# Kernel tuning notes

Hardware: AMD Instinct MI355X
Metric: run time of the kernel (lower is better)

The kernel has to match this reference:

```python
import jax, jax.numpy as jnp
import numpy as np

E, D_IN, H, D_OUT = 8, 6, 32, 2
B = 1048576

def setup_inputs() -> dict:
    key = jax.random.key(0)
    ks = jax.random.split(key, 11)
    s = lambda *sh: 1.0 / np.sqrt(sh[-2])  # glorot-ish scale
    x = jax.random.normal(ks[0], (B, D_IN), dtype=jnp.float32)
    # stacked expert weights
    W1 = jax.random.normal(ks[1], (E, D_IN, H), dtype=jnp.float32) * (1.0/np.sqrt(D_IN))
    b1 = jnp.zeros((E, H), dtype=jnp.float32)
    W2 = jax.random.normal(ks[2], (E, H, H), dtype=jnp.float32) * (1.0/np.sqrt(H))
    b2 = jnp.zeros((E, H), dtype=jnp.float32)
    W3 = jax.random.normal(ks[3], (E, H, D_OUT), dtype=jnp.float32) * (1.0/np.sqrt(H))
    b3 = jnp.zeros((E, D_OUT), dtype=jnp.float32)
    # gating network
    Wg1 = jax.random.normal(ks[4], (D_IN, H), dtype=jnp.float32) * (1.0/np.sqrt(D_IN))
    bg1 = jnp.zeros((H,), dtype=jnp.float32)
    Wg2 = jax.random.normal(ks[5], (H, E), dtype=jnp.float32) * (1.0/np.sqrt(H))
    bg2 = jnp.zeros((E,), dtype=jnp.float32)
    return {"x": x, "W1": W1, "b1": b1, "W2": W2, "b2": b2, "W3": W3, "b3": b3,
            "Wg1": Wg1, "bg1": bg1, "Wg2": Wg2, "bg2": bg2}

def reference(x, W1, b1, W2, b2, W3, b3, Wg1, bg1, Wg2, bg2):
    # gate: [B, E] softmax probs
    g = jax.nn.softmax(jax.nn.relu(x @ Wg1 + bg1) @ Wg2 + bg2, axis=-1)
    # all experts as batched GEMMs: h1, h2 [B, E, H]; y [B, E, 2]
    h1 = jax.nn.relu(jnp.einsum('bd,edh->beh', x, W1) + b1)
    h2 = jax.nn.relu(jnp.einsum('beh,ehk->bek', h1, W2) + b2)
    y = jnp.einsum('beh,eho->beo', h2, W3) + b3
    # gate-weighted sum over experts -> [B, 2]
    return jnp.einsum('be,beo->bo', g, y)
```

## Files before the change

kernel.cpp:

```cpp
#include <hip/hip_runtime.h>


typedef _Float16 half2_t __attribute__((ext_vector_type(2)));
typedef _Float16 half4_t __attribute__((ext_vector_type(4)));
typedef _Float16 half8_t __attribute__((ext_vector_type(8)));
typedef __fp16   fp16v2  __attribute__((ext_vector_type(2)));
typedef float  float4_t __attribute__((ext_vector_type(4)));
typedef float  float2_t __attribute__((ext_vector_type(2)));
typedef int    int2_t   __attribute__((ext_vector_type(2)));
typedef int    int4_t   __attribute__((ext_vector_type(4)));

#define MFMA_K32(A, B, C) __builtin_amdgcn_mfma_f32_16x16x32_f16((A), (B), (C), 0, 0, 0)
#define MFMA_K16(A, B, C) __builtin_amdgcn_mfma_f32_16x16x16f16((A), (B), (C), 0, 0, 0)

static constexpr int E_ = 8, DIN_ = 6, H_ = 32, EPW_ = 2;

union H8U { half2_t h2[4]; half8_t h8; int4_t i4; };
union H4U { half2_t h2[2]; half4_t h4; int2_t i2; };
union HI  { half2_t h; int i; };
union PKU { fp16v2 p; half2_t h; };
union FI  { float f; int i; };

__device__ __forceinline__ half2_t pkrtz(float a, float b) {
    PKU u; u.p = __builtin_amdgcn_cvt_pkrtz(a, b);
    return u.h;
}

__device__ __forceinline__ half2_t relu2(half2_t v) {
    const half2_t z = {(_Float16)0.0f, (_Float16)0.0f};
    return __builtin_elementwise_max(v, z);
}

__device__ __forceinline__ float bperm_f(int addr, float v) {
    FI u; u.f = v;
    u.i = __builtin_amdgcn_ds_bpermute(addr, u.i);
    return u.f;
}

__global__ __launch_bounds__(256, 2)
void moe_kernel(
    const float* __restrict__ x,  const float* __restrict__ W1, const float* __restrict__ b1,
    const float* __restrict__ W2, const float* __restrict__ b2, const float* __restrict__ W3,
    const float* __restrict__ b3, const float* __restrict__ Wg1, const float* __restrict__ bg1,
    const float* __restrict__ Wg2, const float* __restrict__ bg2,
    float* __restrict__ out, int nTiles, int tilesPerBlock)
{
    const int tid  = threadIdx.x;
    const int lane = tid & 63;
    const int t    = lane & 15;
    const int q    = lane >> 4;
    const int wv   = tid >> 6;
    const int eb   = wv * EPW_;

    __shared__ float2_t cbuf[2][4][16];

    const float L2E = 1.44269504f;

    H4U G1[2];
    #pragma unroll
    for (int f = 0; f < 2; ++f) {
        float v0 = 0.f, v1 = 0.f, v2 = 0.f, v3 = 0.f;
        if (q == 0) {
            v0 = Wg1[0 * H_ + f * 16 + t]; v1 = Wg1[1 * H_ + f * 16 + t];
            v2 = Wg1[2 * H_ + f * 16 + t]; v3 = Wg1[3 * H_ + f * 16 + t];
        } else if (q == 1) {
            v0 = Wg1[4 * H_ + f * 16 + t]; v1 = Wg1[5 * H_ + f * 16 + t];
            v2 = bg1[f * 16 + t];          v3 = 0.f;
        }
        G1[f].h2[0] = pkrtz(v0, v1); G1[f].h2[1] = pkrtz(v2, v3);
    }
    H8U G2;
    #pragma unroll
    for (int p = 0; p < 4; ++p) {
        int c0 = ((p >> 1) << 4) + q * 4 + ((p & 1) << 1);
        float v0 = (t < E_) ? Wg2[c0 * E_ + t] * L2E : 0.f;
        float v1 = (t < E_) ? Wg2[(c0 + 1) * E_ + t] * L2E : 0.f;
        G2.h2[p] = pkrtz(v0, v1);
    }

    H4U W1F[EPW_][2];
    H8U W2F[EPW_][2], W3F[EPW_], B2R[EPW_];
    #pragma unroll
    for (int j = 0; j < EPW_; ++j) {
        const int e = eb + j;
        #pragma unroll
        for (int f = 0; f < 2; ++f) {
            float v0 = 0.f, v1 = 0.f, v2 = 0.f, v3 = 0.f;
            const float* We = W1 + (size_t)e * DIN_ * H_ + f * 16 + t;
            if (q == 0)      { v0 = We[0 * H_]; v1 = We[1 * H_]; v2 = We[2 * H_]; v3 = We[3 * H_]; }
            else if (q == 1) { v0 = We[4 * H_]; v1 = We[5 * H_]; v2 = b1[e * H_ + f * 16 + t]; }
            W1F[j][f].h2[0] = pkrtz(v0, v1); W1F[j][f].h2[1] = pkrtz(v2, v3);
        }
        #pragma unroll
        for (int p = 0; p < 4; ++p) {
            int c0 = ((p >> 1) << 4) + q * 4 + ((p & 1) << 1);
            W2F[j][0].h2[p] = pkrtz(W2[(e * H_ + c0) * H_ + 0  + t], W2[(e * H_ + c0 + 1) * H_ + 0  + t]);
            W2F[j][1].h2[p] = pkrtz(W2[(e * H_ + c0) * H_ + 16 + t], W2[(e * H_ + c0 + 1) * H_ + 16 + t]);
            B2R[j].h2[p]    = pkrtz(b2[e * H_ + c0], b2[e * H_ + c0 + 1]);
            float v0 = 0.f, v1 = 0.f;
            if ((t >> 1) == e) {
                v0 = W3[(e * H_ + c0) * 2 + (t & 1)];
                v1 = W3[(e * H_ + c0 + 1) * 2 + (t & 1)];
            }
            W3F[j].h2[p] = pkrtz(v0, v1);
        }
    }

    float4_t bg2F, b3F;
    #pragma unroll
    for (int r = 0; r < 4; ++r) {
        int m = q * 4 + r;
        bg2F[r] = (m < E_) ? bg2[m] * L2E : 0.f;
        b3F[r]  = b3[m];
    }
    const float4_t zero4 = {0.f, 0.f, 0.f, 0.f};

    const int gsrc = ((((q >> 1) << 4) | t) << 2);
    const int csrc = (((wv << 4) | t) << 2);

    const int tile0 = blockIdx.x * tilesPerBlock;

    const int xo1 = (q == 0) ? 0 : 4;
    const int xo2 = (q == 0) ? 2 : 4;
    const float* xq = x + ((size_t)tile0 * 16 + t) * DIN_;
    float2_t la = {0.f, 0.f}, lb = {0.f, 0.f};
    if (tile0 < nTiles) {
        la = *(const float2_t*)(xq + xo1);
        lb = *(const float2_t*)(xq + xo2);
    }

    HI onei; onei.h = pkrtz(1.f, 0.f);
    const bool isq0 = (q == 0);

    for (int it = 0; it < tilesPerBlock; ++it) {
        const int tile = tile0 + it;
        if (tile >= nTiles) break;

        H4U ux;
        ux.h2[0] = pkrtz(la[0], la[1]);
        HI hb; hb.h = pkrtz(lb[0], lb[1]);
        HI se; se.i = isq0 ? hb.i : onei.i;
        ux.h2[1] = se.h;
        const half4_t xB = ux.h4;

        if ((it + 1) < tilesPerBlock && (tile + 1) < nTiles) {
            const float* xn = xq + (size_t)(it + 1) * 16 * DIN_;
            la = *(const float2_t*)(xn + xo1);
            lb = *(const float2_t*)(xn + xo2);
        }

        float4_t hgLo = MFMA_K16(G1[0].h4, xB, zero4);
        float4_t hgHi = MFMA_K16(G1[1].h4, xB, zero4);
        H8U uh;
        uh.h2[0] = relu2(pkrtz(hgLo[0], hgLo[1]));
        uh.h2[1] = relu2(pkrtz(hgLo[2], hgLo[3]));
        uh.h2[2] = relu2(pkrtz(hgHi[0], hgHi[1]));
        uh.h2[3] = relu2(pkrtz(hgHi[2], hgHi[3]));
        float4_t gl = MFMA_K32(G2.h8, uh.h8, bg2F);

        float ex0 = __builtin_amdgcn_exp2f(gl[0]);
        float ex1 = __builtin_amdgcn_exp2f(gl[1]);
        float ex2 = __builtin_amdgcn_exp2f(gl[2]);
        float ex3 = __builtin_amdgcn_exp2f(gl[3]);
        float s = (ex0 + ex1) + (ex2 + ex3);
        s += __shfl_xor(s, 16);
        float rs = __builtin_amdgcn_rcpf(s);
        HI pa, pb;
        pa.h = pkrtz(ex0, ex1);
        pb.h = pkrtz(ex2, ex3);
        int va = __builtin_amdgcn_ds_bpermute(gsrc, pa.i);
        int vb = __builtin_amdgcn_ds_bpermute(gsrc, pb.i);
        HI gsel; gsel.i = (q & 1) ? vb : va;
        float ga = (float)gsel.h[0];
        float gb = (float)gsel.h[1];

        float4_t Y = b3F;
        #pragma unroll
        for (int j = 0; j < EPW_; ++j) {
            float4_t lo = MFMA_K16(W1F[j][0].h4, xB, zero4);
            float4_t hi = MFMA_K16(W1F[j][1].h4, xB, zero4);
            H8U u1;
            u1.h2[0] = relu2(pkrtz(lo[0], lo[1]));
            u1.h2[1] = relu2(pkrtz(lo[2], lo[3]));
            u1.h2[2] = relu2(pkrtz(hi[0], hi[1]));
            u1.h2[3] = relu2(pkrtz(hi[2], hi[3]));
            float4_t lo2 = MFMA_K32(W2F[j][0].h8, u1.h8, zero4);
            float4_t hi2 = MFMA_K32(W2F[j][1].h8, u1.h8, zero4);
            H8U u2;
            u2.h2[0] = relu2(pkrtz(lo2[0], lo2[1]) + B2R[j].h2[0]);
            u2.h2[1] = relu2(pkrtz(lo2[2], lo2[3]) + B2R[j].h2[1]);
            u2.h2[2] = relu2(pkrtz(hi2[0], hi2[1]) + B2R[j].h2[2]);
            u2.h2[3] = relu2(pkrtz(hi2[2], hi2[3]) + B2R[j].h2[3]);
            Y = MFMA_K32(W3F[j].h8, u2.h8, Y);
        }

        float p0 = ga * Y[0] + gb * Y[2];
        float p1 = ga * Y[1] + gb * Y[3];
        p0 = bperm_f(csrc, p0);
        p1 = bperm_f(csrc, p1);

        if (lane < 16) {
            float2_t o = {p0, p1};
            cbuf[it & 1][wv][t] = o;
        }
        __syncthreads();
        if (wv == 0 && lane < 16) {
            float2_t o  = cbuf[it & 1][0][t];
            float2_t o1 = cbuf[it & 1][1][t];
            float2_t o2 = cbuf[it & 1][2][t];
            float2_t o3 = cbuf[it & 1][3][t];
            o[0] = (o[0] + o1[0] + o2[0] + o3[0]) * rs;
            o[1] = (o[1] + o1[1] + o2[1] + o3[1]) * rs;
            *(float2_t*)(out + ((size_t)tile * 16 + t) * 2) = o;
        }
    }
}

extern "C" void kernel_launch(void* const* d_in, const int* in_sizes, int n_in,
                              void* d_out, int out_size, void* d_ws, size_t ws_size,
                              hipStream_t stream) {
    const float* x   = (const float*)d_in[0];
    const float* W1  = (const float*)d_in[1];
    const float* b1  = (const float*)d_in[2];
    const float* W2  = (const float*)d_in[3];
    const float* b2  = (const float*)d_in[4];
    const float* W3  = (const float*)d_in[5];
    const float* b3  = (const float*)d_in[6];
    const float* Wg1 = (const float*)d_in[7];
    const float* bg1 = (const float*)d_in[8];
    const float* Wg2 = (const float*)d_in[9];
    const float* bg2 = (const float*)d_in[10];
    float* out = (float*)d_out;

    const int B      = in_sizes[0] / DIN_;
    const int nTiles = (B + 15) / 16;
    const int blocks = 2048;
    const int tpb    = (nTiles + blocks - 1) / blocks;

    moe_kernel<<<blocks, 256, 0, stream>>>(x, W1, b1, W2, b2, W3, b3,
                                           Wg1, bg1, Wg2, bg2, out, nTiles, tpb);
}
```

Measured before the change: 155.3 us.

## Split experts across block pairs, combine results with atomics instead of LDS sync

Each wave now handles four experts and its own range of tiles, with odd and even blocks covering the two expert halves. This replaces the per-tile __syncthreads and LDS cross-wave reduction with shuffle reductions plus an atomicAdd into an output zeroed by a memset. Softmax normalisation moves before the per-expert weighting. In exchange, each token's gate network and x load are computed twice, register pressure rises from holding four experts' weights per wave, and a memset plus float atomics are added.

Result: slower. 185.7 us (+19.5%).

```diff
diff --git a/kernel.cpp b/kernel.cpp
--- a/kernel.cpp
+++ b/kernel.cpp
@@ -13,13 +13,12 @@
 #define MFMA_K32(A, B, C) __builtin_amdgcn_mfma_f32_16x16x32_f16((A), (B), (C), 0, 0, 0)
 #define MFMA_K16(A, B, C) __builtin_amdgcn_mfma_f32_16x16x16f16((A), (B), (C), 0, 0, 0)
 
-static constexpr int E_ = 8, DIN_ = 6, H_ = 32, EPW_ = 2;
+static constexpr int E_ = 8, DIN_ = 6, H_ = 32, EPH_ = 4;
 
 union H8U { half2_t h2[4]; half8_t h8; int4_t i4; };
 union H4U { half2_t h2[2]; half4_t h4; int2_t i2; };
 union HI  { half2_t h; int i; };
 union PKU { fp16v2 p; half2_t h; };
-union FI  { float f; int i; };
 
 __device__ __forceinline__ half2_t pkrtz(float a, float b) {
     PKU u; u.p = __builtin_amdgcn_cvt_pkrtz(a, b);
@@ -31,32 +30,26 @@
     return __builtin_elementwise_max(v, z);
 }
 
-__device__ __forceinline__ float bperm_f(int addr, float v) {
-    FI u; u.f = v;
-    u.i = __builtin_amdgcn_ds_bpermute(addr, u.i);
-    return u.f;
-}
-
-__global__ __launch_bounds__(256, 2)
+__global__ __launch_bounds__(256)
 void moe_kernel(
     const float* __restrict__ x,  const float* __restrict__ W1, const float* __restrict__ b1,
     const float* __restrict__ W2, const float* __restrict__ b2, const float* __restrict__ W3,
     const float* __restrict__ b3, const float* __restrict__ Wg1, const float* __restrict__ bg1,
     const float* __restrict__ Wg2, const float* __restrict__ bg2,
-    float* __restrict__ out, int nTiles, int tilesPerBlock)
+    float* __restrict__ out, int nTiles, int tilesPerWave)
 {
     const int tid  = threadIdx.x;
     const int lane = tid & 63;
     const int t    = lane & 15;
     const int q    = lane >> 4;
-    const int wv   = tid >> 6;
-    const int eb   = wv * EPW_;
-
-    __shared__ float2_t cbuf[2][4][16];
+    const int half_= blockIdx.x & 1;
+    const int wid  = (int)(((blockIdx.x >> 1) * blockDim.x + tid) >> 6);
+    const int eb   = half_ * EPH_;
 
     const float L2E = 1.44269504f;
 
     H4U G1[2];
+    H8U G2;
     #pragma unroll
     for (int f = 0; f < 2; ++f) {
         float v0 = 0.f, v1 = 0.f, v2 = 0.f, v3 = 0.f;
@@ -69,7 +62,6 @@
         }
         G1[f].h2[0] = pkrtz(v0, v1); G1[f].h2[1] = pkrtz(v2, v3);
     }
-    H8U G2;
     #pragma unroll
     for (int p = 0; p < 4; ++p) {
         int c0 = ((p >> 1) << 4) + q * 4 + ((p & 1) << 1);
@@ -78,10 +70,10 @@
         G2.h2[p] = pkrtz(v0, v1);
     }
 
-    H4U W1F[EPW_][2];
-    H8U W2F[EPW_][2], W3F[EPW_], B2R[EPW_];
-    #pragma unroll
-    for (int j = 0; j < EPW_; ++j) {
+    H4U W1F[EPH_][2];
+    H8U W2F[EPH_][2], W3F[EPH_], B2R[EPH_];
+    #pragma unroll
+    for (int j = 0; j < EPH_; ++j) {
         const int e = eb + j;
         #pragma unroll
         for (int f = 0; f < 2; ++f) {
@@ -111,18 +103,19 @@
     for (int r = 0; r < 4; ++r) {
         int m = q * 4 + r;
         bg2F[r] = (m < E_) ? bg2[m] * L2E : 0.f;
-        b3F[r]  = b3[m];
+        b3F[r]  = ((q >> 1) == half_) ? b3[m] : 0.f;
     }
     const float4_t zero4 = {0.f, 0.f, 0.f, 0.f};
 
     const int gsrc = ((((q >> 1) << 4) | t) << 2);
-    const int csrc = (((wv << 4) | t) << 2);
-
-    const int tile0 = blockIdx.x * tilesPerBlock;
+
+    const int tile0 = wid * tilesPerWave;
 
     const int xo1 = (q == 0) ? 0 : 4;
     const int xo2 = (q == 0) ? 2 : 4;
     const float* xq = x + ((size_t)tile0 * 16 + t) * DIN_;
+    const int strideT = 16 * DIN_;
+
     float2_t la = {0.f, 0.f}, lb = {0.f, 0.f};
     if (tile0 < nTiles) {
         la = *(const float2_t*)(xq + xo1);
@@ -132,9 +125,12 @@
     HI onei; onei.h = pkrtz(1.f, 0.f);
     const bool isq0 = (q == 0);
 
-    for (int it = 0; it < tilesPerBlock; ++it) {
+    const int osel = (lane >> 4) & 1;
+
+    for (int it = 0; it < tilesPerWave; ++it) {
         const int tile = tile0 + it;
         if (tile >= nTiles) break;
+        const int tok = tile * 16 + t;
 
         H4U ux;
         ux.h2[0] = pkrtz(la[0], la[1]);
@@ -143,8 +139,8 @@
         ux.h2[1] = se.h;
         const half4_t xB = ux.h4;
 
-        if ((it + 1) < tilesPerBlock && (tile + 1) < nTiles) {
-            const float* xn = xq + (size_t)(it + 1) * 16 * DIN_;
+        if ((it + 1) < tilesPerWave && (tile + 1) < nTiles) {
+            const float* xn = xq + (size_t)(it + 1) * strideT;
             la = *(const float2_t*)(xn + xo1);
             lb = *(const float2_t*)(xn + xo2);
         }
@@ -166,8 +162,8 @@
         s += __shfl_xor(s, 16);
         float rs = __builtin_amdgcn_rcpf(s);
         HI pa, pb;
-        pa.h = pkrtz(ex0, ex1);
-        pb.h = pkrtz(ex2, ex3);
+        pa.h = pkrtz(ex0 * rs, ex1 * rs);
+        pb.h = pkrtz(ex2 * rs, ex3 * rs);
         int va = __builtin_amdgcn_ds_bpermute(gsrc, pa.i);
         int vb = __builtin_amdgcn_ds_bpermute(gsrc, pb.i);
         HI gsel; gsel.i = (q & 1) ? vb : va;
@@ -176,7 +172,7 @@
 
         float4_t Y = b3F;
         #pragma unroll
-        for (int j = 0; j < EPW_; ++j) {
+        for (int j = 0; j < EPH_; ++j) {
             float4_t lo = MFMA_K16(W1F[j][0].h4, xB, zero4);
             float4_t hi = MFMA_K16(W1F[j][1].h4, xB, zero4);
             H8U u1;
@@ -196,22 +192,13 @@
 
         float p0 = ga * Y[0] + gb * Y[2];
         float p1 = ga * Y[1] + gb * Y[3];
-        p0 = bperm_f(csrc, p0);
-        p1 = bperm_f(csrc, p1);
-
-        if (lane < 16) {
-            float2_t o = {p0, p1};
-            cbuf[it & 1][wv][t] = o;
-        }
-        __syncthreads();
-        if (wv == 0 && lane < 16) {
-            float2_t o  = cbuf[it & 1][0][t];
-            float2_t o1 = cbuf[it & 1][1][t];
-            float2_t o2 = cbuf[it & 1][2][t];
-            float2_t o3 = cbuf[it & 1][3][t];
-            o[0] = (o[0] + o1[0] + o2[0] + o3[0]) * rs;
-            o[1] = (o[1] + o1[1] + o2[1] + o3[1]) * rs;
-            *(float2_t*)(out + ((size_t)tile * 16 + t) * 2) = o;
+        p0 += __shfl_xor(p0, 16);
+        p0 += __shfl_xor(p0, 32);
+        p1 += __shfl_xor(p1, 16);
+        p1 += __shfl_xor(p1, 32);
+
+        if (lane < 32) {
+            atomicAdd(out + (size_t)tok * 2 + osel, osel ? p1 : p0);
         }
     }
 }
@@ -235,8 +222,10 @@
     const int B      = in_sizes[0] / DIN_;
     const int nTiles = (B + 15) / 16;
     const int blocks = 2048;
-    const int tpb    = (nTiles + blocks - 1) / blocks;
-
+    const int nWavesH = (blocks / 2) * (256 / 64);
+    const int tpw    = (nTiles + nWavesH - 1) / nWavesH;
+
+    hipMemsetAsync(out, 0, (size_t)out_size * sizeof(float), stream);
     moe_kernel<<<blocks, 256, 0, stream>>>(x, W1, b1, W2, b2, W3, b3,
-                                           Wg1, bg1, Wg2, bg2, out, nTiles, tpb);
-}
+                                           Wg1, bg1, Wg2, bg2, out, nTiles, tpw);
+}
```
